# Performance work log

Measured on AMD Instinct MI355X. Metric: run time of the kernel, lower is better.

Reference implementation:

```python
import jax, jax.numpy as jnp
import numpy as np

N = 100000
E = 1600000
DIN = 128
DH = 128
DOUT = 32
G = 64
EPS = 1e-5


def setup_inputs() -> dict:
    key = jax.random.key(0)
    ks = jax.random.split(key, 12)
    x = jax.random.normal(ks[0], (N, DIN), dtype=jnp.float32)
    edge_index = jax.random.randint(ks[1], (2, E), 0, N, dtype=jnp.int64)
    batch = jnp.sort(jax.random.randint(ks[2], (N,), 0, G, dtype=jnp.int64))
    # GCNConv weights (glorot-ish) + zero bias
    W1 = jax.random.normal(ks[3], (DIN, DH), dtype=jnp.float32) * (2.0 / (DIN + DH)) ** 0.5
    b1 = jnp.zeros((DH,), jnp.float32)
    W2 = jax.random.normal(ks[4], (DH, DH), dtype=jnp.float32) * (2.0 / (DH + DH)) ** 0.5
    b2 = jnp.zeros((DH,), jnp.float32)
    # BatchNorm affine params
    g1 = jnp.ones((DH,), jnp.float32); be1 = jnp.zeros((DH,), jnp.float32)
    g2 = jnp.ones((DH,), jnp.float32); be2 = jnp.zeros((DH,), jnp.float32)
    # Linear heads: kaiming normal fan_in relu, bias=0.001
    fw1 = jax.random.normal(ks[5], (DH, DH), dtype=jnp.float32) * (2.0 / DH) ** 0.5
    fb1 = jnp.full((DH,), 0.001, jnp.float32)
    fw2 = jax.random.normal(ks[6], (DH, DOUT), dtype=jnp.float32) * (2.0 / DH) ** 0.5
    fb2 = jnp.full((DOUT,), 0.001, jnp.float32)
    return dict(x=x, edge_index=edge_index, batch=batch, W1=W1, b1=b1, W2=W2, b2=b2,
                g1=g1, be1=be1, g2=g2, be2=be2, fw1=fw1, fb1=fb1, fw2=fw2, fb2=fb2)


def _gcn(x, src, dst, dinv, W, b):
    h = x @ W  # [N, F]
    norm = dinv[src] * dinv[dst]  # [E+N]
    agg = jax.ops.segment_sum(h[src] * norm[:, None], dst, num_segments=N)
    return agg + b


def _bn(h, gamma, beta):
    mu = h.mean(axis=0)
    var = h.var(axis=0)  # biased, matches torch BN training mode
    return (h - mu) * jax.lax.rsqrt(var + EPS) * gamma + beta


def reference(x, edge_index, batch, W1, b1, W2, b2, g1, be1, g2, be2, fw1, fb1, fw2, fb2):
    # add self-loops (PyG GCNConv default)
    loops = jnp.arange(N, dtype=edge_index.dtype)
    src = jnp.concatenate([edge_index[0], loops])
    dst = jnp.concatenate([edge_index[1], loops])
    deg = jax.ops.segment_sum(jnp.ones_like(dst, dtype=x.dtype), dst, num_segments=N)
    dinv = jnp.where(deg > 0, jax.lax.rsqrt(deg), 0.0)

    h = jax.nn.relu(_bn(_gcn(x, src, dst, dinv, W1, b1), g1, be1))
    h = jax.nn.relu(_bn(_gcn(h, src, dst, dinv, W2, b2), g2, be2))

    # global mean pool over graph ids
    sums = jax.ops.segment_sum(h, batch, num_segments=G)
    cnt = jax.ops.segment_sum(jnp.ones((N,), h.dtype), batch, num_segments=G)
    pooled = sums / jnp.maximum(cnt, 1.0)[:, None]  # [G, DH]

    z = jax.nn.relu(pooled @ fw1 + fb1)
    return jax.nn.softmax(z @ fw2 + fb2, axis=1)
```

## Files before the change

### kernel.cpp

```cpp
#include <hip/hip_runtime.h>
#include <hip/hip_bf16.h>
#include <stdint.h>

#define NN 100000
#define NE 1600000
#define DH 128
#define DOUT 32
#define NG 64
#define EPS 1e-5f

#define SCAN_BLK 1024
#define SCAN_NB ((NN + SCAN_BLK - 1) / SCAN_BLK)
#define NBUCKET 32

typedef __attribute__((ext_vector_type(8))) unsigned short ushort8;
typedef __attribute__((ext_vector_type(8))) short bfv8;
typedef __attribute__((ext_vector_type(4))) float f32x4;

__device__ __forceinline__ float b2f(unsigned short u) {
    return __uint_as_float(((unsigned int)u) << 16);
}
__device__ __forceinline__ unsigned int f2b(float f) {
    unsigned int u = __float_as_uint(f);
    return (u + 0x7fffu + ((u >> 16) & 1u)) >> 16;
}
__device__ __forceinline__ float blo(unsigned int v) { return __uint_as_float(v << 16); }
__device__ __forceinline__ float bhi(unsigned int v) { return __uint_as_float(v & 0xffff0000u); }


__global__ void k_count(const int* __restrict__ ei_dst, int* __restrict__ cnt) {
    int i = blockIdx.x * blockDim.x + threadIdx.x;
    int stride = gridDim.x * blockDim.x;
    const int4* d4 = reinterpret_cast<const int4*>(ei_dst);
    for (int e = i; e < NE / 4; e += stride) {
        int4 d = d4[e];
        atomicAdd(&cnt[d.x], 1);
        atomicAdd(&cnt[d.y], 1);
        atomicAdd(&cnt[d.z], 1);
        atomicAdd(&cnt[d.w], 1);
    }
}

__global__ void k_gbound(const int* __restrict__ batch, int* __restrict__ first, int* __restrict__ last) {
    int i = blockIdx.x * blockDim.x + threadIdx.x;
    if (i >= NN) return;
    int g = batch[i];
    if (i == 0 || batch[i - 1] != g) first[g] = i;
    if (i == NN - 1 || batch[i + 1] != g) last[g] = i + 1;
}

__global__ void k_scan_partial(const int* __restrict__ cnt, int* __restrict__ bsum) {
    __shared__ int sdata[256];
    int blk = blockIdx.x, t = threadIdx.x;
    int base = blk * SCAN_BLK + t * 4;
    int s = 0;
#pragma unroll
    for (int q = 0; q < 4; q++) { int idx = base + q; if (idx < NN) s += cnt[idx]; }
    sdata[t] = s; __syncthreads();
    for (int o = 128; o; o >>= 1) { if (t < o) sdata[t] += sdata[t + o]; __syncthreads(); }
    if (t == 0) bsum[blk] = sdata[0];
}

__global__ void k_scan_top(const int* __restrict__ bsum, int* __restrict__ bscan, int* __restrict__ rowptr,
                           const int* __restrict__ first, const int* __restrict__ last, int* __restrict__ gcnt) {
    __shared__ int sd[128];
    int t = threadIdx.x;
    int v = (t < SCAN_NB) ? bsum[t] : 0;
    sd[t] = v; __syncthreads();
    for (int o = 1; o < 128; o <<= 1) {
        int add = (t >= o) ? sd[t - o] : 0;
        __syncthreads();
        sd[t] += add;
        __syncthreads();
    }
    if (t < SCAN_NB) bscan[t] = sd[t] - v;
    if (t == 127) rowptr[NN] = sd[127];
    if (t < NG) gcnt[t] = last[t] - first[t];
}

__global__ void k_scan_final(int* __restrict__ cnt, const int* __restrict__ bscan,
                             int* __restrict__ rowptr, float* __restrict__ dinv) {
    __shared__ int sdata[256];
    int blk = blockIdx.x, t = threadIdx.x;
    int base = blk * SCAN_BLK + t * 4;
    int v[4]; int s = 0;
#pragma unroll
    for (int q = 0; q < 4; q++) { int idx = base + q; v[q] = (idx < NN) ? cnt[idx] : 0; s += v[q]; }
    sdata[t] = s; __syncthreads();
    for (int o = 1; o < 256; o <<= 1) {
        int add = (t >= o) ? sdata[t - o] : 0;
        __syncthreads();
        sdata[t] += add;
        __syncthreads();
    }
    int offset = bscan[blk] + sdata[t] - s;
#pragma unroll
    for (int q = 0; q < 4; q++) {
        int idx = base + q;
        if (idx < NN) {
            rowptr[idx] = offset;
            cnt[idx] = offset;
            dinv[idx] = rsqrtf((float)(v[q] + 1));
            offset += v[q];
        }
    }
}

__global__ void k_fill(const int* __restrict__ ei, int* __restrict__ cursor, int* __restrict__ csr) {
    int i = blockIdx.x * blockDim.x + threadIdx.x;
    int stride = gridDim.x * blockDim.x;
    const int4* s4 = reinterpret_cast<const int4*>(ei);
    const int4* d4 = reinterpret_cast<const int4*>(ei + NE);
    for (int e = i; e < NE / 4; e += stride) {
        int4 s = s4[e];
        int4 d = d4[e];
        csr[atomicAdd(&cursor[d.x], 1)] = s.x;
        csr[atomicAdd(&cursor[d.y], 1)] = s.y;
        csr[atomicAdd(&cursor[d.z], 1)] = s.z;
        csr[atomicAdd(&cursor[d.w], 1)] = s.w;
    }
}


__global__ void k_prepw(const float* __restrict__ W1, const float* __restrict__ W2,
                        unsigned short* __restrict__ WT1, unsigned short* __restrict__ WT2) {
    int i = blockIdx.x * blockDim.x + threadIdx.x;
    int sel = i >> 14;
    int j = i & 16383;
    int k = j >> 7, n = j & 127;
    const float* W = sel ? W2 : W1;
    unsigned short* WT = sel ? WT2 : WT1;
    WT[n * 128 + k] = (unsigned short)f2b(W[j]);
}


template <bool BN, typename AT>
__global__ __launch_bounds__(256) void k_gemm(const AT* __restrict__ A, const unsigned short* __restrict__ WTg,
                                              unsigned short* __restrict__ C, const float* __restrict__ rowscale,
                                              const float* __restrict__ scale, const float* __restrict__ shift) {
    __shared__ unsigned char lds[65536];
    unsigned char* As = lds;
    unsigned char* Ws = lds + 32768;
    int row0 = blockIdx.x * 128;
    int t = threadIdx.x;
    int l = t & 63;
    int w = t >> 6;

    if constexpr (sizeof(AT) == 4) {
#pragma unroll
        for (int q = 0; q < 16; q++) {
            int idx = q * 256 + t;
            int r = idx >> 5, c4 = idx & 31;
            float4 v = make_float4(0.f, 0.f, 0.f, 0.f);
            if (row0 + r < NN) v = reinterpret_cast<const float4*>(A)[(size_t)(row0 + r) * 32 + c4];
            ushort4 u;
            u.x = (unsigned short)f2b(v.x);
            u.y = (unsigned short)f2b(v.y);
            u.z = (unsigned short)f2b(v.z);
            u.w = (unsigned short)f2b(v.w);
            int off = r * 256 + ((c4 * 8) ^ ((r & 7) << 4));
            *reinterpret_cast<ushort4*>(As + off) = u;
        }
    } else {
#pragma unroll
        for (int q = 0; q < 8; q++) {
            int idx = q * 256 + t;
            int r = idx >> 4, c8 = idx & 15;
            ushort8 v = (ushort8)0;
            if (row0 + r < NN) v = reinterpret_cast<const ushort8*>(A)[(size_t)(row0 + r) * 16 + c8];
            ushort8 u;
#pragma unroll
            for (int j = 0; j < 8; j++) {
                float f = b2f(v[j]);
                if (BN) { int k = c8 * 8 + j; f = fmaxf(f * scale[k] + shift[k], 0.f); }
                u[j] = (unsigned short)f2b(f);
            }
            int off = r * 256 + ((c8 * 16) ^ ((r & 7) << 4));
            *reinterpret_cast<ushort8*>(As + off) = u;
        }
    }
#pragma unroll
    for (int q = 0; q < 8; q++) {
        int idx = q * 256 + t;
        int n = idx >> 4, c8 = idx & 15;
        ushort8 v = reinterpret_cast<const ushort8*>(WTg)[idx];
        int off = n * 256 + ((c8 * 16) ^ ((n & 7) << 4));
        *reinterpret_cast<ushort8*>(Ws + off) = v;
    }
    __syncthreads();

    f32x4 acc[2][8];
#pragma unroll
    for (int m = 0; m < 2; m++)
#pragma unroll
        for (int n = 0; n < 8; n++) acc[m][n] = (f32x4)0.f;

    int lrow = l & 15;
    int kbyte0 = (l >> 4) * 16;
#pragma unroll
    for (int kt = 0; kt < 4; kt++) {
        int kb = kt * 64 + kbyte0;
        bfv8 a[2];
#pragma unroll
        for (int m = 0; m < 2; m++) {
            int r = w * 32 + m * 16 + lrow;
            a[m] = *reinterpret_cast<const bfv8*>(As + r * 256 + (kb ^ ((r & 7) << 4)));
        }
        bfv8 b[8];
#pragma unroll
        for (int n = 0; n < 8; n++) {
            int r = n * 16 + lrow;
            b[n] = *reinterpret_cast<const bfv8*>(Ws + r * 256 + (kb ^ ((r & 7) << 4)));
        }
#pragma unroll
        for (int m = 0; m < 2; m++)
#pragma unroll
            for (int n = 0; n < 8; n++)
                acc[m][n] = __builtin_amdgcn_mfma_f32_16x16x32_bf16(a[m], b[n], acc[m][n], 0, 0, 0);
    }

#pragma unroll
    for (int m = 0; m < 2; m++) {
#pragma unroll
        for (int rr = 0; rr < 4; rr++) {
            int grow = row0 + w * 32 + m * 16 + (l >> 4) * 4 + rr;
            if (grow < NN) {
                float rs = rowscale[grow];
#pragma unroll
                for (int n = 0; n < 8; n++) {
                    int col = n * 16 + (l & 15);
                    C[(size_t)grow * DH + col] = (unsigned short)f2b(acc[m][n][rr] * rs);
                }
            }
        }
    }
}


__global__ __launch_bounds__(128) void k_aggregate(const unsigned short* __restrict__ h, const int* __restrict__ rowptr,
                                                   const int* __restrict__ csr, const float* __restrict__ dinv,
                                                   unsigned short* __restrict__ agg, float* __restrict__ stats) {
    int lane = threadIdx.x & 63;
    int wv = threadIdx.x >> 6;
    int half = lane >> 5;
    int sl = lane & 31;
    const uint2* h64 = reinterpret_cast<const uint2*>(h);
    uint2* agg64 = reinterpret_cast<uint2*>(agg);
    int wid = blockIdx.x * 2 + wv;
    int nw = gridDim.x * 2;
    long long tlo = ((long long)wid * NE) / nw;
    long long thi = (wid == nw - 1) ? (long long)NE + 1 : (((long long)(wid + 1) * NE) / nw);

    int lo = 0, hi = NN;
    while (lo < hi) {
        int mid = (lo + hi) >> 1;
        if (rowptr[mid] < (int)tlo) lo = mid + 1; else hi = mid;
    }

    float s0 = 0.f, s1 = 0.f, s2 = 0.f, s3 = 0.f;
    float q0 = 0.f, q1 = 0.f, q2 = 0.f, q3 = 0.f;
    for (int i = lo; i < NN; i++) {
        int row = rowptr[i];
        if (row >= (int)thi) break;
        int end = rowptr[i + 1];
        int len = end - row;
        float di = dinv[i];
        float a0 = 0.f, a1 = 0.f, a2 = 0.f, a3 = 0.f;
        if (half == 0) {
            uint2 sv = h64[(size_t)i * 32 + sl];
            a0 = blo(sv.x); a1 = bhi(sv.x); a2 = blo(sv.y); a3 = bhi(sv.y);
        }
        int hc = (len + 1 - half) >> 1;
        int tt = 0;
        for (; tt + 4 <= hc; tt += 4) {
            int eA = row + (tt << 1) + half;
            int n0 = csr[eA], n1 = csr[eA + 2], n2 = csr[eA + 4], n3 = csr[eA + 6];
            uint2 v0 = h64[(size_t)n0 * 32 + sl];
            uint2 v1 = h64[(size_t)n1 * 32 + sl];
            uint2 v2 = h64[(size_t)n2 * 32 + sl];
            uint2 v3 = h64[(size_t)n3 * 32 + sl];
            a0 += blo(v0.x); a1 += bhi(v0.x); a2 += blo(v0.y); a3 += bhi(v0.y);
            a0 += blo(v1.x); a1 += bhi(v1.x); a2 += blo(v1.y); a3 += bhi(v1.y);
            a0 += blo(v2.x); a1 += bhi(v2.x); a2 += blo(v2.y); a3 += bhi(v2.y);
            a0 += blo(v3.x); a1 += bhi(v3.x); a2 += blo(v3.y); a3 += bhi(v3.y);
        }
        for (; tt < hc; tt++) {
            int e = row + (tt << 1) + half;
            int n = csr[e];
            uint2 v = h64[(size_t)n * 32 + sl];
            a0 += blo(v.x); a1 += bhi(v.x); a2 += blo(v.y); a3 += bhi(v.y);
        }
        a0 += __shfl_xor(a0, 32);
        a1 += __shfl_xor(a1, 32);
        a2 += __shfl_xor(a2, 32);
        a3 += __shfl_xor(a3, 32);
        a0 *= di; a1 *= di; a2 *= di; a3 *= di;
        if (half == 0) {
            uint2 o;
            o.x = f2b(a0) | (f2b(a1) << 16);
            o.y = f2b(a2) | (f2b(a3) << 16);
            agg64[(size_t)i * 32 + sl] = o;
            s0 += a0; q0 += a0 * a0;
            s1 += a1; q1 += a1 * a1;
            s2 += a2; q2 += a2 * a2;
            s3 += a3; q3 += a3 * a3;
        }
    }
    if (half == 0) {
        float* b = stats + (size_t)(wid & (NBUCKET - 1)) * 256;
        atomicAdd(&b[sl * 4 + 0], s0);
        atomicAdd(&b[sl * 4 + 1], s1);
        atomicAdd(&b[sl * 4 + 2], s2);
        atomicAdd(&b[sl * 4 + 3], s3);
        atomicAdd(&b[128 + sl * 4 + 0], q0);
        atomicAdd(&b[128 + sl * 4 + 1], q1);
        atomicAdd(&b[128 + sl * 4 + 2], q2);
        atomicAdd(&b[128 + sl * 4 + 3], q3);
    }
}

__global__ void k_bnparams(const float* __restrict__ stats, const float* __restrict__ gamma,
                           const float* __restrict__ beta, float* __restrict__ scale, float* __restrict__ shift) {
    int j = threadIdx.x;
    float su = 0.f, sq = 0.f;
    for (int b = 0; b < NBUCKET; b++) { su += stats[b * 256 + j]; sq += stats[b * 256 + 128 + j]; }
    float mu = su * (1.f / NN);
    float var = sq * (1.f / NN) - mu * mu;
    float rs = rsqrtf(var + EPS);
    float sc = rs * gamma[j];
    scale[j] = sc;
    shift[j] = beta[j] - mu * sc;
}


#define POOL_CHUNK 64

__global__ __launch_bounds__(64) void k_pool(const unsigned short* __restrict__ agg, const int* __restrict__ batch,
                                             const float* __restrict__ scale, const float* __restrict__ shift,
                                             float* __restrict__ pooled) {
    int j = threadIdx.x;
    const unsigned int* a32 = reinterpret_cast<const unsigned int*>(agg);
    int n0 = blockIdx.x * POOL_CHUNK;
    int n1 = n0 + POOL_CHUNK; if (n1 > NN) n1 = NN;
    float sc0 = scale[j * 2], sh0 = shift[j * 2];
    float sc1 = scale[j * 2 + 1], sh1 = shift[j * 2 + 1];
    int gcur = batch[n0];
    float acc0 = 0.f, acc1 = 0.f;
    for (int i = n0; i < n1; i++) {
        int g = batch[i];
        if (g != gcur) {
            atomicAdd(&pooled[(size_t)gcur * DH + j * 2], acc0);
            atomicAdd(&pooled[(size_t)gcur * DH + j * 2 + 1], acc1);
            acc0 = acc1 = 0.f; gcur = g;
        }
        unsigned int v = a32[(size_t)i * 64 + j];
        acc0 += fmaxf(blo(v) * sc0 + sh0, 0.f);
        acc1 += fmaxf(bhi(v) * sc1 + sh1, 0.f);
    }
    atomicAdd(&pooled[(size_t)gcur * DH + j * 2], acc0);
    atomicAdd(&pooled[(size_t)gcur * DH + j * 2 + 1], acc1);
}


__global__ __launch_bounds__(128) void k_head(const float* __restrict__ pooled, const int* __restrict__ gcnt,
                                              const float* __restrict__ fw1, const float* __restrict__ fb1,
                                              const float* __restrict__ fw2, const float* __restrict__ fb2,
                                              float* __restrict__ out) {
    __shared__ float p[DH];
    __shared__ float z[DH];
    int g = blockIdx.x;
    int j = threadIdx.x;
    float cnt = (float)max(gcnt[g], 1);
    p[j] = pooled[(size_t)g * DH + j] / cnt;
    __syncthreads();
    float a = fb1[j];
    for (int k = 0; k < DH; k++) a += p[k] * fw1[k * DH + j];
    z[j] = fmaxf(a, 0.f);
    __syncthreads();
    if (j < DOUT) {
        float l = fb2[j];
        for (int k = 0; k < DH; k++) l += z[k] * fw2[k * DOUT + j];
        float m = l;
        for (int o = 16; o; o >>= 1) m = fmaxf(m, __shfl_xor(m, o, 32));
        float e = expf(l - m);
        float s = e;
        for (int o = 16; o; o >>= 1) s += __shfl_xor(s, o, 32);
        out[(size_t)g * DOUT + j] = e / s;
    }
}


static inline char* align256p(char* p) {
    return (char*)(((uintptr_t)p + 255) & ~(uintptr_t)255);
}

extern "C" void kernel_launch(void* const* d_in, const int* in_sizes, int n_in,
                              void* d_out, int out_size, void* d_ws, size_t ws_size,
                              hipStream_t stream) {
    const float* x     = (const float*)d_in[0];
    const int*   ei    = (const int*)d_in[1];
    const int*   batch = (const int*)d_in[2];
    const float* W1    = (const float*)d_in[3];
    const float* W2    = (const float*)d_in[5];
    const float* g1    = (const float*)d_in[7];
    const float* be1   = (const float*)d_in[8];
    const float* g2    = (const float*)d_in[9];
    const float* be2   = (const float*)d_in[10];
    const float* fw1   = (const float*)d_in[11];
    const float* fb1   = (const float*)d_in[12];
    const float* fw2   = (const float*)d_in[13];
    const float* fb2   = (const float*)d_in[14];
    float* out = (float*)d_out;

    char* w = (char*)d_ws;
    unsigned short* hbuf = (unsigned short*)w;  w += (size_t)NN * DH * 2;
    unsigned short* abuf = (unsigned short*)w;  w += (size_t)NN * DH * 2;
    int*   csr    = (int*)w;    w += (size_t)NE * 4;
    int*   rowptr = (int*)w;    w += (size_t)(NN + 1) * 4;  w = align256p(w);
    float* dinv   = (float*)w;  w += (size_t)NN * 4;
    int*   bsum   = (int*)w;    w += 512 * 4;
    int*   bscan  = (int*)w;    w += 512 * 4;
    float* scale1 = (float*)w;  w += DH * 4;
    float* shift1 = (float*)w;  w += DH * 4;
    float* scale2 = (float*)w;  w += DH * 4;
    float* shift2 = (float*)w;  w += DH * 4;
    unsigned short* WT1g = (unsigned short*)w;  w += (size_t)DH * DH * 2;
    unsigned short* WT2g = (unsigned short*)w;  w += (size_t)DH * DH * 2;
    w = align256p(w);
    char* zstart  = w;
    int*   cnt    = (int*)w;    w += (size_t)NN * 4;
    int*   gfirst = (int*)w;    w += 64 * 4;
    int*   glast  = (int*)w;    w += 64 * 4;
    int*   gcnt   = (int*)w;    w += 64 * 4;
    float* stats1 = (float*)w;  w += (size_t)NBUCKET * 256 * 4;
    float* stats2 = (float*)w;  w += (size_t)NBUCKET * 256 * 4;
    float* pooled = (float*)w;  w += (size_t)NG * DH * 4;
    size_t zbytes = (size_t)(w - zstart);
    size_t need = (size_t)(w - (char*)d_ws);
    if (ws_size < need) return;

    hipMemsetAsync(zstart, 0, zbytes, stream);

    k_prepw<<<128, 256, 0, stream>>>(W1, W2, WT1g, WT2g);
    k_count<<<1024, 256, 0, stream>>>(ei + NE, cnt);
    k_gbound<<<(NN + 255) / 256, 256, 0, stream>>>(batch, gfirst, glast);
    k_scan_partial<<<SCAN_NB, 256, 0, stream>>>(cnt, bsum);
    k_scan_top<<<1, 128, 0, stream>>>(bsum, bscan, rowptr, gfirst, glast, gcnt);
    k_scan_final<<<SCAN_NB, 256, 0, stream>>>(cnt, bscan, rowptr, dinv);
    k_fill<<<1024, 256, 0, stream>>>(ei, cnt, csr);

    int gemm_grid = (NN + 127) / 128;

    k_gemm<false, float><<<gemm_grid, 256, 0, stream>>>(x, WT1g, hbuf, dinv, nullptr, nullptr);
    k_aggregate<<<4096, 128, 0, stream>>>(hbuf, rowptr, csr, dinv, abuf, stats1);
    k_bnparams<<<1, 128, 0, stream>>>(stats1, g1, be1, scale1, shift1);

    k_gemm<true, unsigned short><<<gemm_grid, 256, 0, stream>>>(abuf, WT2g, hbuf, dinv, scale1, shift1);
    k_aggregate<<<4096, 128, 0, stream>>>(hbuf, rowptr, csr, dinv, abuf, stats2);
    k_bnparams<<<1, 128, 0, stream>>>(stats2, g2, be2, scale2, shift2);

    int pool_grid = (NN + POOL_CHUNK - 1) / POOL_CHUNK;
    k_pool<<<pool_grid, 64, 0, stream>>>(abuf, batch, scale2, shift2, pooled);
    k_head<<<NG, 128, 0, stream>>>(pooled, gcnt, fw1, fb1, fw2, fb2, out);
}
```

Before: 469.6 us.

## Partition CSR build atomics by node range, add nontemporal hints, deepen aggregate unroll

k_count and k_fill now split blocks into four groups, each scanning all edges but only doing atomics for destinations in its own quarter of the node range. The intent is to localize atomic traffic in cache, at the cost of reading the edge list four times. Edge, CSR-index and aggregate output accesses now use nontemporal loads and stores. The aggregate kernel unrolls its gather loop to 8 neighbors for more loads in flight, and launches 256-thread blocks with half as many blocks, keeping the same total wave count.

```diff
diff --git a/kernel.cpp b/kernel.cpp
--- a/kernel.cpp
+++ b/kernel.cpp
@@ -12,10 +12,14 @@
 #define SCAN_BLK 1024
 #define SCAN_NB ((NN + SCAN_BLK - 1) / SCAN_BLK)
 #define NBUCKET 32
+#define NRANGE 4
+#define RANGE_SZ (NN / NRANGE)
 
 typedef __attribute__((ext_vector_type(8))) unsigned short ushort8;
 typedef __attribute__((ext_vector_type(8))) short bfv8;
 typedef __attribute__((ext_vector_type(4))) float f32x4;
+typedef __attribute__((ext_vector_type(4))) int intv4;
+typedef __attribute__((ext_vector_type(2))) unsigned int uintv2;
 
 __device__ __forceinline__ float b2f(unsigned short u) {
     return __uint_as_float(((unsigned int)u) << 16);
@@ -29,15 +33,34 @@
 
 
 __global__ void k_count(const int* __restrict__ ei_dst, int* __restrict__ cnt) {
-    int i = blockIdx.x * blockDim.x + threadIdx.x;
-    int stride = gridDim.x * blockDim.x;
-    const int4* d4 = reinterpret_cast<const int4*>(ei_dst);
+    int range = blockIdx.x & (NRANGE - 1);
+    int lo = range * RANGE_SZ, hi = lo + RANGE_SZ;
+    int i = (blockIdx.x >> 2) * blockDim.x + threadIdx.x;
+    int stride = (gridDim.x >> 2) * blockDim.x;
+    const intv4* d4 = reinterpret_cast<const intv4*>(ei_dst);
     for (int e = i; e < NE / 4; e += stride) {
-        int4 d = d4[e];
-        atomicAdd(&cnt[d.x], 1);
-        atomicAdd(&cnt[d.y], 1);
-        atomicAdd(&cnt[d.z], 1);
-        atomicAdd(&cnt[d.w], 1);
+        intv4 d = __builtin_nontemporal_load(d4 + e);
+        if (d.x >= lo && d.x < hi) atomicAdd(&cnt[d.x], 1);
+        if (d.y >= lo && d.y < hi) atomicAdd(&cnt[d.y], 1);
+        if (d.z >= lo && d.z < hi) atomicAdd(&cnt[d.z], 1);
+        if (d.w >= lo && d.w < hi) atomicAdd(&cnt[d.w], 1);
+    }
+}
+
+__global__ void k_fill(const int* __restrict__ ei, int* __restrict__ cursor, int* __restrict__ csr) {
+    int range = blockIdx.x & (NRANGE - 1);
+    int lo = range * RANGE_SZ, hi = lo + RANGE_SZ;
+    int i = (blockIdx.x >> 2) * blockDim.x + threadIdx.x;
+    int stride = (gridDim.x >> 2) * blockDim.x;
+    const intv4* s4 = reinterpret_cast<const intv4*>(ei);
+    const intv4* d4 = reinterpret_cast<const intv4*>(ei + NE);
+    for (int e = i; e < NE / 4; e += stride) {
+        intv4 s = __builtin_nontemporal_load(s4 + e);
+        intv4 d = __builtin_nontemporal_load(d4 + e);
+        if (d.x >= lo && d.x < hi) csr[atomicAdd(&cursor[d.x], 1)] = s.x;
+        if (d.y >= lo && d.y < hi) csr[atomicAdd(&cursor[d.y], 1)] = s.y;
+        if (d.z >= lo && d.z < hi) csr[atomicAdd(&cursor[d.z], 1)] = s.z;
+        if (d.w >= lo && d.w < hi) csr[atomicAdd(&cursor[d.w], 1)] = s.w;
     }
 }
 
@@ -103,21 +126,6 @@
             dinv[idx] = rsqrtf((float)(v[q] + 1));
             offset += v[q];
         }
-    }
-}
-
-__global__ void k_fill(const int* __restrict__ ei, int* __restrict__ cursor, int* __restrict__ csr) {
-    int i = blockIdx.x * blockDim.x + threadIdx.x;
-    int stride = gridDim.x * blockDim.x;
-    const int4* s4 = reinterpret_cast<const int4*>(ei);
-    const int4* d4 = reinterpret_cast<const int4*>(ei + NE);
-    for (int e = i; e < NE / 4; e += stride) {
-        int4 s = s4[e];
-        int4 d = d4[e];
-        csr[atomicAdd(&cursor[d.x], 1)] = s.x;
-        csr[atomicAdd(&cursor[d.y], 1)] = s.y;
-        csr[atomicAdd(&cursor[d.z], 1)] = s.z;
-        csr[atomicAdd(&cursor[d.w], 1)] = s.w;
     }
 }
 
@@ -237,17 +245,17 @@
 }
 
 
-__global__ __launch_bounds__(128) void k_aggregate(const unsigned short* __restrict__ h, const int* __restrict__ rowptr,
+__global__ __launch_bounds__(256) void k_aggregate(const unsigned short* __restrict__ h, const int* __restrict__ rowptr,
                                                    const int* __restrict__ csr, const float* __restrict__ dinv,
                                                    unsigned short* __restrict__ agg, float* __restrict__ stats) {
     int lane = threadIdx.x & 63;
     int wv = threadIdx.x >> 6;
     int half = lane >> 5;
     int sl = lane & 31;
-    const uint2* h64 = reinterpret_cast<const uint2*>(h);
-    uint2* agg64 = reinterpret_cast<uint2*>(agg);
-    int wid = blockIdx.x * 2 + wv;
-    int nw = gridDim.x * 2;
+    const uintv2* h64 = reinterpret_cast<const uintv2*>(h);
+    uintv2* agg64 = reinterpret_cast<uintv2*>(agg);
+    int wid = blockIdx.x * 4 + wv;
+    int nw = gridDim.x * 4;
     long long tlo = ((long long)wid * NE) / nw;
     long long thi = (wid == nw - 1) ? (long long)NE + 1 : (((long long)(wid + 1) * NE) / nw);
 
@@ -267,27 +275,57 @@
         float di = dinv[i];
         float a0 = 0.f, a1 = 0.f, a2 = 0.f, a3 = 0.f;
         if (half == 0) {
-            uint2 sv = h64[(size_t)i * 32 + sl];
+            uintv2 sv = h64[(size_t)i * 32 + sl];
             a0 = blo(sv.x); a1 = bhi(sv.x); a2 = blo(sv.y); a3 = bhi(sv.y);
         }
         int hc = (len + 1 - half) >> 1;
         int tt = 0;
-        for (; tt + 4 <= hc; tt += 4) {
+        for (; tt + 8 <= hc; tt += 8) {
             int eA = row + (tt << 1) + half;
-            int n0 = csr[eA], n1 = csr[eA + 2], n2 = csr[eA + 4], n3 = csr[eA + 6];
-            uint2 v0 = h64[(size_t)n0 * 32 + sl];
-            uint2 v1 = h64[(size_t)n1 * 32 + sl];
-            uint2 v2 = h64[(size_t)n2 * 32 + sl];
-            uint2 v3 = h64[(size_t)n3 * 32 + sl];
+            int n0 = __builtin_nontemporal_load(&csr[eA]);
+            int n1 = __builtin_nontemporal_load(&csr[eA + 2]);
+            int n2 = __builtin_nontemporal_load(&csr[eA + 4]);
+            int n3 = __builtin_nontemporal_load(&csr[eA + 6]);
+            int n4 = __builtin_nontemporal_load(&csr[eA + 8]);
+            int n5 = __builtin_nontemporal_load(&csr[eA + 10]);
+            int n6 = __builtin_nontemporal_load(&csr[eA + 12]);
+            int n7 = __builtin_nontemporal_load(&csr[eA + 14]);
+            uintv2 v0 = h64[(size_t)n0 * 32 + sl];
+            uintv2 v1 = h64[(size_t)n1 * 32 + sl];
+            uintv2 v2 = h64[(size_t)n2 * 32 + sl];
+            uintv2 v3 = h64[(size_t)n3 * 32 + sl];
+            uintv2 v4 = h64[(size_t)n4 * 32 + sl];
+            uintv2 v5 = h64[(size_t)n5 * 32 + sl];
+            uintv2 v6 = h64[(size_t)n6 * 32 + sl];
+            uintv2 v7 = h64[(size_t)n7 * 32 + sl];
             a0 += blo(v0.x); a1 += bhi(v0.x); a2 += blo(v0.y); a3 += bhi(v0.y);
             a0 += blo(v1.x); a1 += bhi(v1.x); a2 += blo(v1.y); a3 += bhi(v1.y);
             a0 += blo(v2.x); a1 += bhi(v2.x); a2 += blo(v2.y); a3 += bhi(v2.y);
             a0 += blo(v3.x); a1 += bhi(v3.x); a2 += blo(v3.y); a3 += bhi(v3.y);
+            a0 += blo(v4.x); a1 += bhi(v4.x); a2 += blo(v4.y); a3 += bhi(v4.y);
+            a0 += blo(v5.x); a1 += bhi(v5.x); a2 += blo(v5.y); a3 += bhi(v5.y);
+            a0 += blo(v6.x); a1 += bhi(v6.x); a2 += blo(v6.y); a3 += bhi(v6.y);
+            a0 += blo(v7.x); a1 += bhi(v7.x); a2 += blo(v7.y); a3 += bhi(v7.y);
+        }
+        for (; tt + 4 <= hc; tt += 4) {
+            int eA = row + (tt << 1) + half;
+            int n0 = __builtin_nontemporal_load(&csr[eA]);
+            int n1 = __builtin_nontemporal_load(&csr[eA + 2]);
+            int n2 = __builtin_nontemporal_load(&csr[eA + 4]);
+            int n3 = __builtin_nontemporal_load(&csr[eA + 6]);
+            uintv2 v0 = h64[(size_t)n0 * 32 + sl];
+            uintv2 v1 = h64[(size_t)n1 * 32 + sl];
+            uintv2 v2 = h64[(size_t)n2 * 32 + sl];
+            uintv2 v3 = h64[(size_t)n3 * 32 + sl];
+            a0 += blo(v0.x); a1 += bhi(v0.x); a2 += blo(v0.y); a3 += bhi(v0.y);
+            a0 += blo(v1.x); a1 += bhi(v1.x); a2 += blo(v1.y); a3 += bhi(v1.y);
+            a0 += blo(v2.x); a1 += bhi(v2.x); a2 += blo(v2.y); a3 += bhi(v2.y);
+            a0 += blo(v3.x); a1 += bhi(v3.x); a2 += blo(v3.y); a3 += bhi(v3.y);
         }
         for (; tt < hc; tt++) {
             int e = row + (tt << 1) + half;
-            int n = csr[e];
-            uint2 v = h64[(size_t)n * 32 + sl];
+            int n = __builtin_nontemporal_load(&csr[e]);
+            uintv2 v = h64[(size_t)n * 32 + sl];
             a0 += blo(v.x); a1 += bhi(v.x); a2 += blo(v.y); a3 += bhi(v.y);
         }
         a0 += __shfl_xor(a0, 32);
@@ -296,10 +334,10 @@
         a3 += __shfl_xor(a3, 32);
         a0 *= di; a1 *= di; a2 *= di; a3 *= di;
         if (half == 0) {
-            uint2 o;
+            uintv2 o;
             o.x = f2b(a0) | (f2b(a1) << 16);
             o.y = f2b(a2) | (f2b(a3) << 16);
-            agg64[(size_t)i * 32 + sl] = o;
+            __builtin_nontemporal_store(o, agg64 + ((size_t)i * 32 + sl));
             s0 += a0; q0 += a0 * a0;
             s1 += a1; q1 += a1 * a1;
             s2 += a2; q2 += a2 * a2;
@@ -452,11 +490,11 @@
     int gemm_grid = (NN + 127) / 128;
 
     k_gemm<false, float><<<gemm_grid, 256, 0, stream>>>(x, WT1g, hbuf, dinv, nullptr, nullptr);
-    k_aggregate<<<4096, 128, 0, stream>>>(hbuf, rowptr, csr, dinv, abuf, stats1);
+    k_aggregate<<<2048, 256, 0, stream>>>(hbuf, rowptr, csr, dinv, abuf, stats1);
     k_bnparams<<<1, 128, 0, stream>>>(stats1, g1, be1, scale1, shift1);
 
     k_gemm<true, unsigned short><<<gemm_grid, 256, 0, stream>>>(abuf, WT2g, hbuf, dinv, scale1, shift1);
-    k_aggregate<<<4096, 128, 0, stream>>>(hbuf, rowptr, csr, dinv, abuf, stats2);
+    k_aggregate<<<2048, 256, 0, stream>>>(hbuf, rowptr, csr, dinv, abuf, stats2);
     k_bnparams<<<1, 128, 0, stream>>>(stats2, g2, be2, scale2, shift2);
 
     int pool_grid = (NN + POOL_CHUNK - 1) / POOL_CHUNK;
```

After: 503.6 us. 1.07x slower.
